# Kernel optimization log

Hardware: AMD Instinct MI355X
Metric: run time of the kernel (lower is better)

## Reference

```python
import jax, jax.numpy as jnp
import numpy as np

N_PEDS = 4096
GRID_N = 16          # grid is GRID_N x GRID_N cells
CELL_SIDE = 0.6      # meters per cell
POOL_DIM = 2         # DIRECTIONAL pooling: relative (vx, vy)
OUT_DIM = 256
H_DIM = 128
AREA = 20.0          # scene is AREA x AREA meters


def setup_inputs() -> dict:
    key = jax.random.key(0)
    k1, k2, k3, k4, k5 = jax.random.split(key, 5)
    positions = jax.random.uniform(k1, (N_PEDS, 2), dtype=jnp.float32) * AREA
    # past position = current minus a small per-step displacement (~pedestrian velocity)
    past_positions = positions - jax.random.normal(k2, (N_PEDS, 2), dtype=jnp.float32) * 0.4
    h = jax.random.normal(k3, (N_PEDS, H_DIM), dtype=jnp.float32)
    in_dim = GRID_N * GRID_N * POOL_DIM
    scale = 1.0 / np.sqrt(in_dim)
    W_emb = jax.random.uniform(k4, (OUT_DIM, in_dim), dtype=jnp.float32, minval=-scale, maxval=scale)
    b_emb = jax.random.uniform(k5, (OUT_DIM,), dtype=jnp.float32, minval=-scale, maxval=scale)
    return {"h": h, "positions": positions, "past_positions": past_positions,
            "W_emb": W_emb, "b_emb": b_emb}


def _directional_grid(positions, past_positions):
    """DIRECTIONAL grid pooling: bin neighbours' relative velocities into an
    n x n grid (cell_side meters per cell) centred on each pedestrian, averaging
    contributions per cell (norm_cell=True). Returns [N, n*n, 2]."""
    n = GRID_N
    num = positions.shape[0]
    vel = positions - past_positions                         # [N, 2]
    rel_pos = positions[None, :, :] - positions[:, None, :]  # [N, N, 2] pos_j - pos_i
    rel_vel = vel[None, :, :] - vel[:, None, :]              # [N, N, 2] vel_j - vel_i
    # cell indices: floor(rel/cell + n/2)
    oij = jnp.floor(rel_pos / CELL_SIDE + n / 2).astype(jnp.int32)  # [N, N, 2]
    in_range = jnp.all((oij >= 0) & (oij < n), axis=-1)             # [N, N]
    valid = in_range & ~jnp.eye(num, dtype=bool)                    # exclude self
    cell_idx = jnp.where(valid, oij[..., 0] * n + oij[..., 1], 0)   # [N, N]
    vals = jnp.where(valid[..., None], rel_vel, 0.0)                # [N, N, 2]
    rows = jnp.arange(num)[:, None]                                 # [N, 1]
    grid = jnp.zeros((num, n * n, POOL_DIM), dtype=positions.dtype)
    grid = grid.at[rows, cell_idx].add(vals)                        # scatter-add values
    cnt = jnp.zeros((num, n * n), dtype=positions.dtype)
    cnt = cnt.at[rows, cell_idx].add(valid.astype(positions.dtype)) # occupancy counts
    grid = grid / jnp.maximum(cnt, 1.0)[..., None]                  # norm_cell: mean per cell
    return grid


def reference(h, positions, past_positions, W_emb, b_emb):
    grid = _directional_grid(positions, past_positions)      # [N, n*n, 2]
    flat = grid.reshape(grid.shape[0], -1)                   # [N, n*n*2]
    return jax.nn.relu(flat @ W_emb.T + b_emb)               # [N, out_dim]
```

## Files before the change

### kernel.cpp

```cpp
#include <hip/hip_runtime.h>

typedef __attribute__((ext_vector_type(4))) float f32x4;
typedef __attribute__((ext_vector_type(8))) short bf16x8;

#define NP 4096

__device__ __forceinline__ unsigned short f2bf(float f) {
  unsigned int u = __float_as_uint(f);
  u = u + 0x7FFFu + ((u >> 16) & 1u);
  return (unsigned short)(u >> 16);
}

__global__ __launch_bounds__(256, 8) void pool_kernel(
    const float2* __restrict__ pos, const float2* __restrict__ past,
    const float* __restrict__ W, unsigned short* __restrict__ Wb,
    unsigned short* __restrict__ gridws) {
  __shared__ unsigned long long acc[4][256];
  const int tid = threadIdx.x;
  const int b = blockIdx.x;
  const int ibase = (b & 7) * 512 + (b >> 3) * 4;

  if (tid < 16) {
    int idx = b * 128 + tid * 8;
    float4 w0 = *(const float4*)&W[idx];
    float4 w1 = *(const float4*)&W[idx + 4];
    bf16x8 bv;
    bv[0] = (short)f2bf(w0.x); bv[1] = (short)f2bf(w0.y);
    bv[2] = (short)f2bf(w0.z); bv[3] = (short)f2bf(w0.w);
    bv[4] = (short)f2bf(w1.x); bv[5] = (short)f2bf(w1.y);
    bv[6] = (short)f2bf(w1.z); bv[7] = (short)f2bf(w1.w);
    *(bf16x8*)&Wb[idx] = bv;
  }

  for (int idx = tid; idx < 1024; idx += 256)
    ((unsigned long long*)acc)[idx] = 0ull;
  __syncthreads();

  float2 pip[4];
  float vix[4], viy[4];
#pragma unroll
  for (int t = 0; t < 4; ++t) {
    float2 p = pos[ibase + t];
    float2 q = past[ibase + t];
    pip[t] = p;
    vix[t] = p.x - q.x;
    viy[t] = p.y - q.y;
  }
  const float inv06 = 1.0f / 0.6f;

  for (int jo = 0; jo < NP; jo += 256) {
    const int j = jo + tid;
    const float2 pj = pos[j];
    const float2 qj = past[j];
    const float vjx = pj.x - qj.x;
    const float vjy = pj.y - qj.y;
#pragma unroll
    for (int t = 0; t < 4; ++t) {
      float rx = pj.x - pip[t].x;
      float ry = pj.y - pip[t].y;
      float ax = __builtin_fmaf(rx, inv06, 8.0f);
      float ay = __builtin_fmaf(ry, inv06, 8.0f);
      bool unc = (fabsf(ax - rintf(ax)) < 1e-4f) |
                 (fabsf(ay - rintf(ay)) < 1e-4f);
      float fx, fy;
      if (__any(unc)) {
        fx = floorf(rx / 0.6f + 8.0f);
        fy = floorf(ry / 0.6f + 8.0f);
      } else {
        fx = floorf(ax);
        fy = floorf(ay);
      }
      int ix = (int)fx;
      int iy = (int)fy;
      if (((unsigned)ix < 16u) & ((unsigned)iy < 16u)) {
        unsigned int qx = (unsigned int)((int)rintf((vjx - vix[t]) * 2048.0f) + 16384);
        unsigned int qy = (unsigned int)((int)rintf((vjy - viy[t]) * 2048.0f) + 16384);
        unsigned long long p = ((unsigned long long)qx << 38) |
                               ((unsigned long long)qy << 12) | 1ull;
        atomicAdd(&acc[t][(ix << 4) + iy], p);
      }
    }
  }
  __syncthreads();

  const int cell = tid;
  const float selfc = (cell == 136) ? 1.0f : 0.0f;
#pragma unroll
  for (int t = 0; t < 4; ++t) {
    unsigned long long raw = acc[t][cell];
    unsigned int cnt = (unsigned int)(raw & 0xFFFull);
    int sxq = (int)((unsigned int)(raw >> 38)) - (int)(cnt << 14);
    int syq = (int)((unsigned int)((raw >> 12) & 0x3FFFFFFull)) - (int)(cnt << 14);
    float cn = (float)cnt - selfc;
    float d = fmaxf(cn, 1.0f);
    float sx = (float)sxq * (1.0f / 2048.0f);
    float sy = (float)syq * (1.0f / 2048.0f);
    unsigned int packed =
        ((unsigned int)f2bf(sy / d) << 16) | (unsigned int)f2bf(sx / d);
    *(unsigned int*)&gridws[(size_t)(ibase + t) * 512 + cell * 2] = packed;
  }
}

__global__ __launch_bounds__(256) void gemm_kernel(
    const unsigned short* __restrict__ A, const unsigned short* __restrict__ Wb,
    const float* __restrict__ bias, float* __restrict__ out) {
  __shared__ float red[4][64][20];
  const int tid = threadIdx.x;
  const int lane = tid & 63;
  const int w = tid >> 6;
  const int g = blockIdx.x;
  const int xcd = g & 7;
  const int idx = g >> 3;
  const int mbase = (xcd * 32 + (idx & 31)) * 16;
  const int nbase = (idx >> 5) * 64;
  const int lrow = lane & 15;
  const int lk8 = (lane >> 4) * 8;

  f32x4 acc[4] = {};
#pragma unroll
  for (int ksp = 0; ksp < 4; ksp += 2) {
    bf16x8 a[2], b[2][4];
#pragma unroll
    for (int u = 0; u < 2; ++u) {
      const int k0 = w * 128 + (ksp + u) * 32 + lk8;
      a[u] = *(const bf16x8*)&A[(size_t)(mbase + lrow) * 512 + k0];
#pragma unroll
      for (int nf = 0; nf < 4; ++nf)
        b[u][nf] = *(const bf16x8*)&Wb[(size_t)(nbase + nf * 16 + lrow) * 512 + k0];
    }
#pragma unroll
    for (int u = 0; u < 2; ++u)
#pragma unroll
      for (int nf = 0; nf < 4; ++nf)
        acc[nf] = __builtin_amdgcn_mfma_f32_16x16x32_bf16(
            a[u], b[u][nf], acc[nf], 0, 0, 0);
  }

  const int rq = (lane >> 4) * 4;
#pragma unroll
  for (int nf = 0; nf < 4; ++nf)
    *(f32x4*)&red[w][nf * 16 + lrow][rq] = acc[nf];
  __syncthreads();

  const int col = tid & 63;
  const int mq = (tid >> 6) * 4;
  f32x4 s = {};
#pragma unroll
  for (int w2 = 0; w2 < 4; ++w2) {
    f32x4 r = *(const f32x4*)&red[w2][col][mq];
    s += r;
  }
  const float bv = bias[nbase + col];
#pragma unroll
  for (int q = 0; q < 4; ++q)
    out[(size_t)(mbase + mq + q) * 256 + nbase + col] = fmaxf(s[q] + bv, 0.0f);
}

extern "C" void kernel_launch(void* const* d_in, const int* in_sizes, int n_in,
                              void* d_out, int out_size, void* d_ws, size_t ws_size,
                              hipStream_t stream) {
  const float2* pos = (const float2*)d_in[1];
  const float2* past = (const float2*)d_in[2];
  const float* W = (const float*)d_in[3];
  const float* bias = (const float*)d_in[4];
  float* out = (float*)d_out;

  unsigned short* gridws = (unsigned short*)d_ws;
  unsigned short* Wb = (unsigned short*)((char*)d_ws + 4 * 1024 * 1024);

  pool_kernel<<<NP / 4, 256, 0, stream>>>(pos, past, W, Wb, gridws);
  gemm_kernel<<<1024, 256, 0, stream>>>(gridws, Wb, bias, out);
}
```

Measured before the change: 34.49 us.

## Pool 8 pedestrians per 512-thread block and split W conversion into own kernel

The pooling kernel now processes 8 target pedestrians per block using 512 threads, so each loaded neighbour j is reused across more targets and the block count halves. The fp32-to-bf16 weight conversion moves out of the pool kernel into a separate small kernel. This reduces redundant global loads of neighbour positions. In exchange it adds a third kernel launch and raises register and LDS pressure per block, which may cut occupancy.

```diff
diff --git a/kernel.cpp b/kernel.cpp
--- a/kernel.cpp
+++ b/kernel.cpp
@@ -4,6 +4,7 @@
 typedef __attribute__((ext_vector_type(8))) short bf16x8;
 
 #define NP 4096
+#define PB 8
 
 __device__ __forceinline__ unsigned short f2bf(float f) {
   unsigned int u = __float_as_uint(f);
@@ -11,53 +12,53 @@
   return (unsigned short)(u >> 16);
 }
 
-__global__ __launch_bounds__(256, 8) void pool_kernel(
+__global__ __launch_bounds__(256) void wconv_kernel(
+    const float* __restrict__ W, unsigned short* __restrict__ Wb) {
+  int i = (blockIdx.x * 256 + threadIdx.x) * 8;
+  float4 w0 = *(const float4*)&W[i];
+  float4 w1 = *(const float4*)&W[i + 4];
+  bf16x8 bv;
+  bv[0] = (short)f2bf(w0.x); bv[1] = (short)f2bf(w0.y);
+  bv[2] = (short)f2bf(w0.z); bv[3] = (short)f2bf(w0.w);
+  bv[4] = (short)f2bf(w1.x); bv[5] = (short)f2bf(w1.y);
+  bv[6] = (short)f2bf(w1.z); bv[7] = (short)f2bf(w1.w);
+  *(bf16x8*)&Wb[i] = bv;
+}
+
+__global__ __launch_bounds__(512, 4) void pool_kernel(
     const float2* __restrict__ pos, const float2* __restrict__ past,
-    const float* __restrict__ W, unsigned short* __restrict__ Wb,
     unsigned short* __restrict__ gridws) {
-  __shared__ unsigned long long acc[4][256];
+  __shared__ unsigned long long acc[PB][256];
   const int tid = threadIdx.x;
   const int b = blockIdx.x;
-  const int ibase = (b & 7) * 512 + (b >> 3) * 4;
+  const int ibase = (b & 7) * 512 + (b >> 3) * PB;
 
-  if (tid < 16) {
-    int idx = b * 128 + tid * 8;
-    float4 w0 = *(const float4*)&W[idx];
-    float4 w1 = *(const float4*)&W[idx + 4];
-    bf16x8 bv;
-    bv[0] = (short)f2bf(w0.x); bv[1] = (short)f2bf(w0.y);
-    bv[2] = (short)f2bf(w0.z); bv[3] = (short)f2bf(w0.w);
-    bv[4] = (short)f2bf(w1.x); bv[5] = (short)f2bf(w1.y);
-    bv[6] = (short)f2bf(w1.z); bv[7] = (short)f2bf(w1.w);
-    *(bf16x8*)&Wb[idx] = bv;
-  }
-
-  for (int idx = tid; idx < 1024; idx += 256)
+  for (int idx = tid; idx < PB * 256; idx += 512)
     ((unsigned long long*)acc)[idx] = 0ull;
   __syncthreads();
 
-  float2 pip[4];
-  float vix[4], viy[4];
+  float pxv[PB], pyv[PB], vix[PB], viy[PB];
 #pragma unroll
-  for (int t = 0; t < 4; ++t) {
+  for (int t = 0; t < PB; ++t) {
     float2 p = pos[ibase + t];
     float2 q = past[ibase + t];
-    pip[t] = p;
+    pxv[t] = p.x;
+    pyv[t] = p.y;
     vix[t] = p.x - q.x;
     viy[t] = p.y - q.y;
   }
   const float inv06 = 1.0f / 0.6f;
 
-  for (int jo = 0; jo < NP; jo += 256) {
+  for (int jo = 0; jo < NP; jo += 512) {
     const int j = jo + tid;
     const float2 pj = pos[j];
     const float2 qj = past[j];
     const float vjx = pj.x - qj.x;
     const float vjy = pj.y - qj.y;
 #pragma unroll
-    for (int t = 0; t < 4; ++t) {
-      float rx = pj.x - pip[t].x;
-      float ry = pj.y - pip[t].y;
+    for (int t = 0; t < PB; ++t) {
+      float rx = pj.x - pxv[t];
+      float ry = pj.y - pyv[t];
       float ax = __builtin_fmaf(rx, inv06, 8.0f);
       float ay = __builtin_fmaf(ry, inv06, 8.0f);
       bool unc = (fabsf(ax - rintf(ax)) < 1e-4f) |
@@ -83,10 +84,12 @@
   }
   __syncthreads();
 
-  const int cell = tid;
+  const int cell = tid & 255;
+  const int tg = (tid >> 8) * 4;
   const float selfc = (cell == 136) ? 1.0f : 0.0f;
 #pragma unroll
-  for (int t = 0; t < 4; ++t) {
+  for (int tt = 0; tt < 4; ++tt) {
+    const int t = tg + tt;
     unsigned long long raw = acc[t][cell];
     unsigned int cnt = (unsigned int)(raw & 0xFFFull);
     int sxq = (int)((unsigned int)(raw >> 38)) - (int)(cnt << 14);
@@ -168,6 +171,7 @@
   unsigned short* gridws = (unsigned short*)d_ws;
   unsigned short* Wb = (unsigned short*)((char*)d_ws + 4 * 1024 * 1024);
 
-  pool_kernel<<<NP / 4, 256, 0, stream>>>(pos, past, W, Wb, gridws);
+  wconv_kernel<<<(256 * 512) / (256 * 8), 256, 0, stream>>>(W, Wb);
+  pool_kernel<<<NP / PB, 512, 0, stream>>>(pos, past, gridws);
   gemm_kernel<<<1024, 256, 0, stream>>>(gridws, Wb, bias, out);
 }
```

Result: slower. 38.92 us (+12.8%).
